# Kernel optimization log

Measured on AMD Instinct MI355X. Metric: run time of the kernel, lower is better.

Reference implementation:

```python
import jax, jax.numpy as jnp
import numpy as np

HIDDEN_DIM = 64
MEMORY_SLOTS = 8
SEQ_LEN = 64
VOCAB_SIZE = 64
B = 524288


def setup_inputs() -> dict:
    key = jax.random.key(0)
    k1, k2, k3, k4, k5, k6 = jax.random.split(key, 6)
    seqs = jax.random.randint(k1, (B, SEQ_LEN), 0, VOCAB_SIZE + 2, dtype=jnp.int64 if jax.config.jax_enable_x64 else jnp.int32)
    query_tok = jax.random.randint(k2, (B,), 0, VOCAB_SIZE + 2, dtype=seqs.dtype)
    embed = jax.random.normal(k3, (VOCAB_SIZE + 2, HIDDEN_DIM), dtype=jnp.float32)
    # torch Linear: y = x @ W.T + b
    W1 = jax.random.normal(k4, (HIDDEN_DIM, HIDDEN_DIM * 2), dtype=jnp.float32) * (1.0 / np.sqrt(HIDDEN_DIM * 2))
    b1 = jnp.zeros((HIDDEN_DIM,), dtype=jnp.float32)
    W2 = jax.random.normal(k5, (VOCAB_SIZE, HIDDEN_DIM), dtype=jnp.float32) * (1.0 / np.sqrt(HIDDEN_DIM))
    b2 = jnp.zeros((VOCAB_SIZE,), dtype=jnp.float32)
    return {"seqs": seqs, "query_tok": query_tok, "embed": embed,
            "W1": W1, "b1": b1, "W2": W2, "b2": b2}


def reference(seqs, query_tok, embed, W1, b1, W2, b2):
    # FIFO of capacity MEMORY_SLOTS over tokens t=0..SEQ_LEN-2 keeps exactly the
    # last MEMORY_SLOTS tokens: positions [SEQ_LEN-1-MEMORY_SLOTS, SEQ_LEN-1).
    win = seqs[:, SEQ_LEN - 1 - MEMORY_SLOTS : SEQ_LEN - 1]        # [B, 8]
    mem_summary = embed[win].mean(axis=1)                          # [B, H]
    q_emb = embed[query_tok]                                       # [B, H]
    h = jnp.concatenate([q_emb, mem_summary], axis=-1)             # [B, 2H]
    h = jax.nn.relu(h @ W1.T + b1)                                 # [B, H]
    logits = h @ W2.T + b2                                         # [B, VOCAB]
    return logits
```

## Files before the change

### kernel.cpp

```cpp
#include <hip/hip_runtime.h>

#define HID 64
#define NTOK 66
#define SEQ 64
#define WIN0 55
#define NW 8
#define LDS_STRIDE 72
#define ITERS 8
#define ROWS_PER_ITER 64

typedef short short8 __attribute__((ext_vector_type(8)));
typedef unsigned short ushort8v __attribute__((ext_vector_type(8)));
typedef unsigned int uint4v __attribute__((ext_vector_type(4)));
typedef float float2v __attribute__((ext_vector_type(2)));
typedef float float4v __attribute__((ext_vector_type(4)));

static __device__ __forceinline__ unsigned short f2bf(float f) {
    union { float f; unsigned u; } v; v.f = f;
    unsigned r = v.u + 0x7FFFu + ((v.u >> 16) & 1u);
    return (unsigned short)(r >> 16);
}
static __device__ __forceinline__ float u2f(unsigned u) {
    union { unsigned u; float f; } v; v.u = u;
    return v.f;
}

__global__ void build_tables(const float* __restrict__ embed,
                             const float* __restrict__ W1,
                             const float* __restrict__ b1,
                             unsigned short* __restrict__ tbl) {
    int b = blockIdx.x;
    int tb = b & 1;
    int t  = b >> 1;
    int n  = threadIdx.x;
    float acc = tb ? 0.0f : b1[n];
    const float* er = embed + t * HID;
    const float* wr = W1 + n * (2 * HID) + tb * HID;
#pragma unroll 8
    for (int k = 0; k < HID; ++k) acc += er[k] * wr[k];
    if (tb) acc *= 0.125f;
    tbl[tb * (NTOK * HID) + t * HID + n] = f2bf(acc);
}

static __device__ __forceinline__ short8 build_hfrag(
    const unsigned short* T_lds, int q, const int* w, int k0c) {
    uint4v tv = *(const uint4v*)(T_lds + q * LDS_STRIDE + k0c);
    float2v acc[4];
#pragma unroll
    for (int i = 0; i < 4; ++i) {
        acc[i].x = u2f(tv[i] << 16);
        acc[i].y = u2f(tv[i] & 0xFFFF0000u);
    }
#pragma unroll
    for (int j = 0; j < NW; ++j) {
        uint4v v2 = *(const uint4v*)(T_lds + NTOK * LDS_STRIDE + w[j] * LDS_STRIDE + k0c);
#pragma unroll
        for (int i = 0; i < 4; ++i) {
            float2v p;
            p.x = u2f(v2[i] << 16);
            p.y = u2f(v2[i] & 0xFFFF0000u);
            acc[i] += p;
        }
    }
    short8 a;
#pragma unroll
    for (int i = 0; i < 4; ++i) {
        a[2 * i]     = (short)f2bf(fmaxf(acc[i].x, 0.0f));
        a[2 * i + 1] = (short)f2bf(fmaxf(acc[i].y, 0.0f));
    }
    return a;
}

__global__ __launch_bounds__(256, 4) void fused_forward(
    const int* __restrict__ seqs,
    const int* __restrict__ qtok,
    const float* __restrict__ W2,
    const float* __restrict__ b2,
    const unsigned short* __restrict__ tbl,
    float* __restrict__ out)
{
    __shared__ unsigned short T_lds[2 * NTOK * LDS_STRIDE];

    int tid  = threadIdx.x;
    int wv   = tid >> 6;
    int l    = tid & 63;
    int lrow = l & 15;
    int lg   = l >> 4;
    int lk8  = lg * 8;

    int row0 = blockIdx.x * (ITERS * ROWS_PER_ITER) + wv * 16 + lrow;

#define LOADT(s, t_) { \
    int row_ = row0 + (t_) * ROWS_PER_ITER; \
    q##s = qtok[row_]; \
    const int* sp_ = seqs + row_ * SEQ + WIN0; \
    _Pragma("unroll") \
    for (int j = 0; j < NW; ++j) w##s[j] = sp_[j]; \
}

#define COMPUTE(s, t_) { \
    short8 a0 = build_hfrag(T_lds, q##s, w##s, lk8); \
    short8 a1 = build_hfrag(T_lds, q##s, w##s, 32 + lk8); \
    float* op = out + (size_t)(row0 + (t_) * ROWS_PER_ITER) * HID; \
    _Pragma("unroll") \
    for (int nt = 0; nt < 4; ++nt) { \
        float4v acc = (float4v)(0.0f); \
        acc = __builtin_amdgcn_mfma_f32_16x16x32_bf16(wfrag[nt][0], a0, acc, 0, 0, 0); \
        acc = __builtin_amdgcn_mfma_f32_16x16x32_bf16(wfrag[nt][1], a1, acc, 0, 0, 0); \
        acc += b2v[nt]; \
        *(float4v*)(op + nt * 16 + lg * 4) = acc; \
    } \
}

    int qA, qB;
    int wA[NW], wB[NW];

    LOADT(A, 0);
    LOADT(B, 1);

    short8  wfrag[4][2];
    float4v b2v[4];
#pragma unroll
    for (int nt = 0; nt < 4; ++nt) {
        b2v[nt] = *(const float4v*)(b2 + nt * 16 + lg * 4);
#pragma unroll
        for (int kc = 0; kc < 2; ++kc) {
            const float* wp = W2 + (nt * 16 + lrow) * HID + kc * 32 + lk8;
            short8 f;
#pragma unroll
            for (int j = 0; j < 8; ++j) f[j] = (short)f2bf(wp[j]);
            wfrag[nt][kc] = f;
        }
    }

    for (int i = tid; i < 2 * NTOK * (HID / 8); i += 256) {
        int tbi = i / (NTOK * 8);
        int rem = i - tbi * (NTOK * 8);
        int t   = rem >> 3;
        int kq  = (rem & 7) << 3;
        *(ushort8v*)(T_lds + tbi * (NTOK * LDS_STRIDE) + t * LDS_STRIDE + kq) =
            *(const ushort8v*)(tbl + tbi * (NTOK * HID) + t * HID + kq);
    }
    __syncthreads();

    COMPUTE(A, 0); LOADT(A, 2);
    COMPUTE(B, 1); LOADT(B, 3);
    COMPUTE(A, 2); LOADT(A, 4);
    COMPUTE(B, 3); LOADT(B, 5);
    COMPUTE(A, 4); LOADT(A, 6);
    COMPUTE(B, 5); LOADT(B, 7);
    COMPUTE(A, 6);
    COMPUTE(B, 7);

#undef LOADT
#undef COMPUTE
}

extern "C" void kernel_launch(void* const* d_in, const int* in_sizes, int n_in,
                              void* d_out, int out_size, void* d_ws, size_t ws_size,
                              hipStream_t stream) {
    const int*   seqs  = (const int*)d_in[0];
    const int*   qtok  = (const int*)d_in[1];
    const float* embed = (const float*)d_in[2];
    const float* W1    = (const float*)d_in[3];
    const float* b1    = (const float*)d_in[4];
    const float* W2    = (const float*)d_in[5];
    const float* b2    = (const float*)d_in[6];
    float* out = (float*)d_out;
    unsigned short* tbl = (unsigned short*)d_ws;

    int B = in_sizes[0] / SEQ;

    build_tables<<<NTOK * 2, HID, 0, stream>>>(embed, W1, b1, tbl);

    int grid = B / (ITERS * ROWS_PER_ITER);
    fused_forward<<<grid, 256, 0, stream>>>(seqs, qtok, W2, b2, tbl, out);
}
```

Baseline: 54.69 us.

## Software-pipeline LDS table gathers ahead of sum/convert and MFMA stages

Splits the per-row hidden-fragment build into separate LDS gather and sum/convert steps and double-buffers the gathered vectors, so the gathers for the next half-fragment or next row tile are issued while the current one is summed and fed to MFMA. This is meant to hide LDS latency behind ALU work. It also folds the output bias into the MFMA accumulator init instead of adding it afterwards. The extra 16 live uint4 registers per thread raise register pressure, which could spill or lower occupancy under launch_bounds(256,4).

```diff
diff --git a/kernel.cpp b/kernel.cpp
--- a/kernel.cpp
+++ b/kernel.cpp
@@ -42,35 +42,6 @@
     tbl[tb * (NTOK * HID) + t * HID + n] = f2bf(acc);
 }
 
-static __device__ __forceinline__ short8 build_hfrag(
-    const unsigned short* T_lds, int q, const int* w, int k0c) {
-    uint4v tv = *(const uint4v*)(T_lds + q * LDS_STRIDE + k0c);
-    float2v acc[4];
-#pragma unroll
-    for (int i = 0; i < 4; ++i) {
-        acc[i].x = u2f(tv[i] << 16);
-        acc[i].y = u2f(tv[i] & 0xFFFF0000u);
-    }
-#pragma unroll
-    for (int j = 0; j < NW; ++j) {
-        uint4v v2 = *(const uint4v*)(T_lds + NTOK * LDS_STRIDE + w[j] * LDS_STRIDE + k0c);
-#pragma unroll
-        for (int i = 0; i < 4; ++i) {
-            float2v p;
-            p.x = u2f(v2[i] << 16);
-            p.y = u2f(v2[i] & 0xFFFF0000u);
-            acc[i] += p;
-        }
-    }
-    short8 a;
-#pragma unroll
-    for (int i = 0; i < 4; ++i) {
-        a[2 * i]     = (short)f2bf(fmaxf(acc[i].x, 0.0f));
-        a[2 * i + 1] = (short)f2bf(fmaxf(acc[i].y, 0.0f));
-    }
-    return a;
-}
-
 __global__ __launch_bounds__(256, 4) void fused_forward(
     const int* __restrict__ seqs,
     const int* __restrict__ qtok,
@@ -98,18 +69,67 @@
     for (int j = 0; j < NW; ++j) w##s[j] = sp_[j]; \
 }
 
-#define COMPUTE(s, t_) { \
-    short8 a0 = build_hfrag(T_lds, q##s, w##s, lk8); \
-    short8 a1 = build_hfrag(T_lds, q##s, w##s, 32 + lk8); \
+#define GATHER8(g, ww, k0c) { \
+    _Pragma("unroll") \
+    for (int j = 0; j < NW; ++j) \
+        (g)[j] = *(const uint4v*)(T_lds + NTOK * LDS_STRIDE + (ww)[j] * LDS_STRIDE + (k0c)); \
+}
+
+#define SUMCVT(aout, g, qq, k0c) { \
+    uint4v t1_ = *(const uint4v*)(T_lds + (qq) * LDS_STRIDE + (k0c)); \
+    float2v acc_[4]; \
+    _Pragma("unroll") \
+    for (int i = 0; i < 4; ++i) { \
+        acc_[i].x = u2f((g)[0][i] << 16); acc_[i].y = u2f((g)[0][i] & 0xFFFF0000u); } \
+    _Pragma("unroll") \
+    for (int j = 1; j < NW; ++j) { \
+        _Pragma("unroll") \
+        for (int i = 0; i < 4; ++i) { \
+            float2v p_; p_.x = u2f((g)[j][i] << 16); p_.y = u2f((g)[j][i] & 0xFFFF0000u); \
+            acc_[i] += p_; } } \
+    _Pragma("unroll") \
+    for (int i = 0; i < 4; ++i) { \
+        float2v p_; p_.x = u2f(t1_[i] << 16); p_.y = u2f(t1_[i] & 0xFFFF0000u); \
+        acc_[i] += p_; } \
+    _Pragma("unroll") \
+    for (int i = 0; i < 4; ++i) { \
+        (aout)[2*i]   = (short)f2bf(fmaxf(acc_[i].x, 0.0f)); \
+        (aout)[2*i+1] = (short)f2bf(fmaxf(acc_[i].y, 0.0f)); } \
+}
+
+#define MFST(t_, A0, A1) { \
     float* op = out + (size_t)(row0 + (t_) * ROWS_PER_ITER) * HID; \
     _Pragma("unroll") \
     for (int nt = 0; nt < 4; ++nt) { \
-        float4v acc = (float4v)(0.0f); \
-        acc = __builtin_amdgcn_mfma_f32_16x16x32_bf16(wfrag[nt][0], a0, acc, 0, 0, 0); \
-        acc = __builtin_amdgcn_mfma_f32_16x16x32_bf16(wfrag[nt][1], a1, acc, 0, 0, 0); \
-        acc += b2v[nt]; \
-        *(float4v*)(op + nt * 16 + lg * 4) = acc; \
-    } \
+        float4v acc = b2v[nt]; \
+        acc = __builtin_amdgcn_mfma_f32_16x16x32_bf16(wfrag[nt][0], A0, acc, 0, 0, 0); \
+        acc = __builtin_amdgcn_mfma_f32_16x16x32_bf16(wfrag[nt][1], A1, acc, 0, 0, 0); \
+        *(float4v*)(op + nt * 16 + lg * 4) = acc; } \
+}
+
+#define ITER_FULL(C, N, t_) { \
+    int qc_ = q##C; \
+    GATHER8(gB_, w##C, 32 + lk8);       \
+    SUMCVT(a0, gA_, qc_, lk8);          \
+    LOADT(C, (t_) + 2);                 \
+    GATHER8(gA_, w##N, lk8);            \
+    SUMCVT(a1, gB_, qc_, 32 + lk8);     \
+    MFST(t_, a0, a1); \
+}
+#define ITER_NOLOAD(C, N, t_) { \
+    int qc_ = q##C; \
+    GATHER8(gB_, w##C, 32 + lk8); \
+    SUMCVT(a0, gA_, qc_, lk8); \
+    GATHER8(gA_, w##N, lk8); \
+    SUMCVT(a1, gB_, qc_, 32 + lk8); \
+    MFST(t_, a0, a1); \
+}
+#define ITER_LAST(C, t_) { \
+    int qc_ = q##C; \
+    GATHER8(gB_, w##C, 32 + lk8); \
+    SUMCVT(a0, gA_, qc_, lk8); \
+    SUMCVT(a1, gB_, qc_, 32 + lk8); \
+    MFST(t_, a0, a1); \
 }
 
     int qA, qB;
@@ -143,17 +163,27 @@
     }
     __syncthreads();
 
-    COMPUTE(A, 0); LOADT(A, 2);
-    COMPUTE(B, 1); LOADT(B, 3);
-    COMPUTE(A, 2); LOADT(A, 4);
-    COMPUTE(B, 3); LOADT(B, 5);
-    COMPUTE(A, 4); LOADT(A, 6);
-    COMPUTE(B, 5); LOADT(B, 7);
-    COMPUTE(A, 6);
-    COMPUTE(B, 7);
+    uint4v gA_[NW], gB_[NW];
+    short8 a0, a1;
+
+    GATHER8(gA_, wA, lk8);
+
+    ITER_FULL(A, B, 0);
+    ITER_FULL(B, A, 1);
+    ITER_FULL(A, B, 2);
+    ITER_FULL(B, A, 3);
+    ITER_FULL(A, B, 4);
+    ITER_FULL(B, A, 5);
+    ITER_NOLOAD(A, B, 6);
+    ITER_LAST(B, 7);
 
 #undef LOADT
-#undef COMPUTE
+#undef GATHER8
+#undef SUMCVT
+#undef MFST
+#undef ITER_FULL
+#undef ITER_NOLOAD
+#undef ITER_LAST
 }
 
 extern "C" void kernel_launch(void* const* d_in, const int* in_sizes, int n_in,
```

New measurement: 139.1 us. 154% more time.
